# Optimization experiments

Hardware: AMD Instinct MI355X
Metric: run time of the kernel (lower is better)

Reference implementation:

```python
import jax, jax.numpy as jnp
import numpy as np

N_SAMPLES = 524288
N_FEATURES = 64
N_GATES = 64
N_OUTPUTS = 8
BASE = N_FEATURES + 2                # X cols + constant-0 col + constant-1 col
MAX_CONN = BASE + N_GATES            # 130
TEMPERATURE = 1.0                    # forward() default
NEG = -1e9                           # mask value for not-yet-available slots


def setup_inputs() -> dict:
    key = jax.random.key(0)
    k1, k2, k3 = jax.random.split(key, 3)
    X = jax.random.uniform(k1, (N_SAMPLES, N_FEATURES), dtype=jnp.float32)
    gate_weights = jax.random.normal(k2, (N_GATES, MAX_CONN), dtype=jnp.float32) * 0.1
    output_weights = jax.random.normal(k3, (N_GATES, N_OUTPUTS), dtype=jnp.float32) * 0.1
    output_scale = jnp.ones((N_OUTPUTS,), dtype=jnp.float32)
    return {"X": X, "gate_weights": gate_weights,
            "output_weights": output_weights, "output_scale": output_scale}


def reference(X, gate_weights, output_weights, output_scale):
    n = X.shape[0]
    # available = [X | zeros | ones | gate slots]; gate slots filled sequentially
    buf = jnp.concatenate([
        X,
        jnp.zeros((n, 1), X.dtype),
        jnp.ones((n, 1), X.dtype),
        jnp.zeros((n, N_GATES), X.dtype),
    ], axis=1)                                            # [N, MAX_CONN]

    # Connection selection is data-independent: softmax over the first
    # (BASE + gate_idx) slots of each gate's weight row, then top-2.
    col_ids = jnp.arange(MAX_CONN)
    avail_mask = col_ids[None, :] < (BASE + jnp.arange(N_GATES))[:, None]
    logits = jnp.where(avail_mask, gate_weights / TEMPERATURE, NEG)
    probs = jax.nn.softmax(logits, axis=1)                # [n_gates, MAX_CONN]
    _, top2 = jax.lax.top_k(probs, 2)                     # [n_gates, 2]

    # Sequential NAND chain over a small fixed number of gates (structural loop).
    gate_outs = []
    for i in range(N_GATES):
        a = buf[:, top2[i, 0]]                            # [N]
        b = buf[:, top2[i, 1]]
        g = 1.0 - a * b                                   # continuous NAND
        gate_outs.append(g)
        buf = buf.at[:, BASE + i].set(g)

    gate_matrix = jnp.stack(gate_outs, axis=1)            # [N, n_gates]
    outputs = (gate_matrix @ output_weights) * output_scale
    return outputs
```

## Files before the change

### kernel.cpp

```cpp
#include <hip/hip_runtime.h>

#define N_SAMPLES 524288
#define N_FEATURES 64
#define N_GATES 64
#define N_OUTPUTS 8
#define BASE_COLS 66
#define MAX_CONN 130

#define SPB 128
#define STR 129

__global__ void topk_prep_kernel(const float* __restrict__ gw, int2* __restrict__ gidx) {
    int i = threadIdx.x;
    if (i >= N_GATES) return;
    const float* w = gw + i * MAX_CONN;
    int avail = BASE_COLS + i;
    float v1 = -1e30f, v2 = -1e30f;
    int i1 = 0, i2 = 0;
    for (int j = 0; j < avail; ++j) {
        float x = w[j];
        if (x > v1) { v2 = v1; i2 = i1; v1 = x; i1 = j; }
        else if (x > v2) { v2 = x; i2 = j; }
    }
    gidx[i] = make_int2(i1, i2);
}

__global__ __launch_bounds__(SPB) void circuit_kernel(
    const float* __restrict__ X,
    const int2*  __restrict__ gidx,
    const float* __restrict__ ow,
    const float* __restrict__ scale,
    float*       __restrict__ out)
{
    __shared__ float buf[MAX_CONN * STR];

    const int t = threadIdx.x;
    const long long s0 = (long long)blockIdx.x * SPB;

    const float4* Xv = (const float4*)(X + s0 * N_FEATURES);
    #pragma unroll
    for (int k = 0; k < 16; ++k) {
        float4 v = Xv[k * SPB + t];
        int f = k * (SPB * 4) + t * 4;
        int c = f & 63;
        int s = f >> 6;
        buf[(c + 0) * STR + s] = v.x;
        buf[(c + 1) * STR + s] = v.y;
        buf[(c + 2) * STR + s] = v.z;
        buf[(c + 3) * STR + s] = v.w;
    }
    buf[64 * STR + t] = 0.0f;
    buf[65 * STR + t] = 1.0f;
    __syncthreads();

    float acc[N_OUTPUTS];
    #pragma unroll
    for (int o = 0; o < N_OUTPUTS; ++o) acc[o] = 0.0f;

    for (int i = 0; i < N_GATES; ++i) {
        int2 p = gidx[i];
        float a = buf[p.x * STR + t];
        float b = buf[p.y * STR + t];
        float g = 1.0f - a * b;
        buf[(BASE_COLS + i) * STR + t] = g;
        #pragma unroll
        for (int o = 0; o < N_OUTPUTS; ++o)
            acc[o] = fmaf(g, ow[i * N_OUTPUTS + o], acc[o]);
    }

    float4 o0, o1;
    o0.x = acc[0] * scale[0]; o0.y = acc[1] * scale[1];
    o0.z = acc[2] * scale[2]; o0.w = acc[3] * scale[3];
    o1.x = acc[4] * scale[4]; o1.y = acc[5] * scale[5];
    o1.z = acc[6] * scale[6]; o1.w = acc[7] * scale[7];
    float4* outv = (float4*)(out + (s0 + t) * N_OUTPUTS);
    outv[0] = o0;
    outv[1] = o1;
}

extern "C" void kernel_launch(void* const* d_in, const int* in_sizes, int n_in,
                              void* d_out, int out_size, void* d_ws, size_t ws_size,
                              hipStream_t stream) {
    const float* X     = (const float*)d_in[0];
    const float* gw    = (const float*)d_in[1];
    const float* ow    = (const float*)d_in[2];
    const float* scale = (const float*)d_in[3];
    float* out = (float*)d_out;

    int2* gidx = (int2*)d_ws;

    topk_prep_kernel<<<1, 64, 0, stream>>>(gw, gidx);

    int blocks = N_SAMPLES / SPB;
    circuit_kernel<<<blocks, SPB, 0, stream>>>(X, gidx, ow, scale, out);
}
```

Before: 252.0 us.

## Pack two samples per thread as half2 and parallelize top-2 selection

The NAND chain now stores gate values as packed half2 in shared memory, so each thread handles two samples with one __hfma2 per gate, and a block covers 256 samples. The top-2 prep runs one wavefront per gate and reduces with shuffles instead of a serial scan on one thread. The aim is to halve LDS traffic per sample, reduce block count, and shorten the prep kernel. In exchange, fp16 storage loses precision across the 64-gate chain and could change the top-2 tie handling or breach the output tolerance.

```diff
diff --git a/kernel.cpp b/kernel.cpp
--- a/kernel.cpp
+++ b/kernel.cpp
@@ -1,4 +1,5 @@
 #include <hip/hip_runtime.h>
+#include <hip/hip_fp16.h>
 
 #define N_SAMPLES 524288
 #define N_FEATURES 64
@@ -7,75 +8,104 @@
 #define BASE_COLS 66
 #define MAX_CONN 130
 
-#define SPB 128
+#define TPB 256
+#define NW 128
 #define STR 129
 
-__global__ void topk_prep_kernel(const float* __restrict__ gw, int2* __restrict__ gidx) {
-    int i = threadIdx.x;
-    if (i >= N_GATES) return;
-    const float* w = gw + i * MAX_CONN;
-    int avail = BASE_COLS + i;
-    float v1 = -1e30f, v2 = -1e30f;
-    int i1 = 0, i2 = 0;
-    for (int j = 0; j < avail; ++j) {
-        float x = w[j];
-        if (x > v1) { v2 = v1; i2 = i1; v1 = x; i1 = j; }
-        else if (x > v2) { v2 = x; i2 = j; }
-    }
-    gidx[i] = make_int2(i1, i2);
+__device__ inline void top2_ins(float x, int j, float& v1, int& i1, float& v2, int& i2) {
+    bool gt1 = (x > v1) || (x == v1 && j < i1);
+    bool gt2 = (x > v2) || (x == v2 && j < i2);
+    if (gt1) { v2 = v1; i2 = i1; v1 = x; i1 = j; }
+    else if (gt2) { v2 = x; i2 = j; }
 }
 
-__global__ __launch_bounds__(SPB) void circuit_kernel(
+__global__ __launch_bounds__(64) void topk_prep_kernel(const float* __restrict__ gw,
+                                                       int2* __restrict__ gidx) {
+    const int i = blockIdx.x;
+    const int l = threadIdx.x;
+    const float* w = gw + i * MAX_CONN;
+    const int avail = BASE_COLS + i;
+
+    float v1 = -1e30f, v2 = -1e30f;
+    int   i1 = 0x7fffffff, i2 = 0x7fffffff;
+    for (int s = 0; s < 3; ++s) {
+        int j = l + 64 * s;
+        if (j < avail) top2_ins(w[j], j, v1, i1, v2, i2);
+    }
+    #pragma unroll
+    for (int d = 1; d < 64; d <<= 1) {
+        float ov1 = __shfl_xor(v1, d);
+        int   oi1 = __shfl_xor(i1, d);
+        float ov2 = __shfl_xor(v2, d);
+        int   oi2 = __shfl_xor(i2, d);
+        top2_ins(ov1, oi1, v1, i1, v2, i2);
+        top2_ins(ov2, oi2, v1, i1, v2, i2);
+    }
+    if (l == 0) gidx[i] = make_int2(i1, i2);
+}
+
+__global__ __launch_bounds__(NW) void circuit_kernel(
     const float* __restrict__ X,
     const int2*  __restrict__ gidx,
     const float* __restrict__ ow,
     const float* __restrict__ scale,
     float*       __restrict__ out)
 {
-    __shared__ float buf[MAX_CONN * STR];
+    __shared__ __half2 buf[MAX_CONN * STR];
 
     const int t = threadIdx.x;
-    const long long s0 = (long long)blockIdx.x * SPB;
+    const long long s0 = (long long)blockIdx.x * TPB;
 
     const float4* Xv = (const float4*)(X + s0 * N_FEATURES);
     #pragma unroll
     for (int k = 0; k < 16; ++k) {
-        float4 v = Xv[k * SPB + t];
-        int f = k * (SPB * 4) + t * 4;
-        int c = f & 63;
-        int s = f >> 6;
-        buf[(c + 0) * STR + s] = v.x;
-        buf[(c + 1) * STR + s] = v.y;
-        buf[(c + 2) * STR + s] = v.z;
-        buf[(c + 3) * STR + s] = v.w;
+        int q  = k * NW + t;
+        int c4 = q & 15;
+        int j  = q >> 4;
+        float4 va = Xv[(2 * j)     * 16 + c4];
+        float4 vb = Xv[(2 * j + 1) * 16 + c4];
+        int c = 4 * c4;
+        buf[(c + 0) * STR + j] = __halves2half2(__float2half(va.x), __float2half(vb.x));
+        buf[(c + 1) * STR + j] = __halves2half2(__float2half(va.y), __float2half(vb.y));
+        buf[(c + 2) * STR + j] = __halves2half2(__float2half(va.z), __float2half(vb.z));
+        buf[(c + 3) * STR + j] = __halves2half2(__float2half(va.w), __float2half(vb.w));
     }
-    buf[64 * STR + t] = 0.0f;
-    buf[65 * STR + t] = 1.0f;
+    buf[64 * STR + t] = __halves2half2(__float2half(0.0f), __float2half(0.0f));
+    buf[65 * STR + t] = __halves2half2(__float2half(1.0f), __float2half(1.0f));
     __syncthreads();
 
-    float acc[N_OUTPUTS];
+    float acc0[N_OUTPUTS], acc1[N_OUTPUTS];
     #pragma unroll
-    for (int o = 0; o < N_OUTPUTS; ++o) acc[o] = 0.0f;
+    for (int o = 0; o < N_OUTPUTS; ++o) { acc0[o] = 0.0f; acc1[o] = 0.0f; }
 
+    const __half2 one2 = __halves2half2(__float2half(1.0f), __float2half(1.0f));
+
+    #pragma unroll
     for (int i = 0; i < N_GATES; ++i) {
         int2 p = gidx[i];
-        float a = buf[p.x * STR + t];
-        float b = buf[p.y * STR + t];
-        float g = 1.0f - a * b;
+        __half2 a = buf[p.x * STR + t];
+        __half2 b = buf[p.y * STR + t];
+        __half2 g = __hfma2(__hneg2(a), b, one2);
         buf[(BASE_COLS + i) * STR + t] = g;
+        float g0 = __low2float(g);
+        float g1 = __high2float(g);
         #pragma unroll
-        for (int o = 0; o < N_OUTPUTS; ++o)
-            acc[o] = fmaf(g, ow[i * N_OUTPUTS + o], acc[o]);
+        for (int o = 0; o < N_OUTPUTS; ++o) {
+            float w = ow[i * N_OUTPUTS + o];
+            acc0[o] = fmaf(g0, w, acc0[o]);
+            acc1[o] = fmaf(g1, w, acc1[o]);
+        }
     }
 
-    float4 o0, o1;
-    o0.x = acc[0] * scale[0]; o0.y = acc[1] * scale[1];
-    o0.z = acc[2] * scale[2]; o0.w = acc[3] * scale[3];
-    o1.x = acc[4] * scale[4]; o1.y = acc[5] * scale[5];
-    o1.z = acc[6] * scale[6]; o1.w = acc[7] * scale[7];
-    float4* outv = (float4*)(out + (s0 + t) * N_OUTPUTS);
-    outv[0] = o0;
-    outv[1] = o1;
+    float sc[N_OUTPUTS];
+    #pragma unroll
+    for (int o = 0; o < N_OUTPUTS; ++o) sc[o] = scale[o];
+
+    float4* outv = (float4*)(out + (s0 + 2 * t) * N_OUTPUTS);
+    outv[0] = make_float4(acc0[0] * sc[0], acc0[1] * sc[1], acc0[2] * sc[2], acc0[3] * sc[3]);
+    outv[1] = make_float4(acc0[4] * sc[4], acc0[5] * sc[5], acc0[6] * sc[6], acc0[7] * sc[7]);
+    outv[2] = make_float4(acc1[0] * sc[0], acc1[1] * sc[1], acc1[2] * sc[2], acc1[3] * sc[3]);
+    outv[3] = make_float4(acc1[4] * sc[4], acc1[5] * sc[5], acc1[6] * sc[6], acc1[7] * sc[7]);
 }
 
 extern "C" void kernel_launch(void* const* d_in, const int* in_sizes, int n_in,
@@ -89,8 +119,8 @@
 
     int2* gidx = (int2*)d_ws;
 
-    topk_prep_kernel<<<1, 64, 0, stream>>>(gw, gidx);
+    topk_prep_kernel<<<N_GATES, 64, 0, stream>>>(gw, gidx);
 
-    int blocks = N_SAMPLES / SPB;
-    circuit_kernel<<<blocks, SPB, 0, stream>>>(X, gidx, ow, scale, out);
+    int blocks = N_SAMPLES / TPB;
+    circuit_kernel<<<blocks, NW, 0, stream>>>(X, gidx, ow, scale, out);
 }
```

Result: faster. 217.3 us (-13.8%).
